# Optimization experiments

Hardware: AMD Instinct MI355X
Metric: run time of the kernel (lower is better)

Reference implementation:

```python
import jax, jax.numpy as jnp
import numpy as np

D_MODEL = 512
NUM_HEADS = 8
D_HEAD = 64
B, T = 8, 1024


def sinusoidal_pos(start, end, d, dtype=jnp.float32):
    # positions start .. end-1, standard sinusoidal encoding, shape (1, end-start, d)
    pos = jnp.arange(start, end, dtype=jnp.float32)[:, None]              # (L,1)
    inv_freq = jnp.exp(-jnp.log(10000.0) * jnp.arange(0, d, 2, dtype=jnp.float32) / d)
    ang = pos * inv_freq[None, :]                                          # (L,d/2)
    pe = jnp.stack([jnp.sin(ang), jnp.cos(ang)], axis=-1).reshape(pos.shape[0], d)
    return pe[None].astype(dtype)                                          # (1,L,d)


def _relative_shift(x):
    # x: (B,H,T,L) -> Transformer-XL shift trick
    b, h, t, l = x.shape
    x = jnp.pad(x, ((0, 0), (0, 0), (0, 0), (1, 0)))                       # (B,H,T,L+1)
    x = x.reshape(b, h, l + 1, t)[:, :, 1:, :].reshape(b, h, t, l)
    return x


def setup_inputs() -> dict:
    key = jax.random.key(0)
    ks = jax.random.split(key, 8)
    hd = NUM_HEADS * D_HEAD
    s_in = 1.0 / np.sqrt(D_MODEL)
    s_out = 1.0 / np.sqrt(hd)
    return {
        "xs": jax.random.normal(ks[0], (B, T, D_MODEL), jnp.float32),
        "mask": jnp.ones((B, T, T), jnp.int32),
        "Wq": jax.random.normal(ks[1], (D_MODEL, hd), jnp.float32) * s_in,
        "Wk": jax.random.normal(ks[2], (D_MODEL, hd), jnp.float32) * s_in,
        "Wv": jax.random.normal(ks[3], (D_MODEL, hd), jnp.float32) * s_in,
        "Wpos": jax.random.normal(ks[4], (D_MODEL, hd), jnp.float32) * s_in,
        "Wout": jax.random.normal(ks[5], (hd, D_MODEL), jnp.float32) * s_out,
        "u_bias": jax.random.normal(ks[6], (NUM_HEADS, D_HEAD), jnp.float32) * 0.02,
        "v_bias": jax.random.normal(ks[7], (NUM_HEADS, D_HEAD), jnp.float32) * 0.02,
    }


def reference(xs, mask, Wq, Wk, Wv, Wpos, Wout, u_bias, v_bias):
    b, t, _ = xs.shape
    scale = 1.0 / np.sqrt(D_HEAD)

    def split_heads(y):  # (B,T,H*dh) -> (B,H,T,dh)
        return y.reshape(b, t, NUM_HEADS, D_HEAD).transpose(0, 2, 1, 3)

    q = split_heads(xs @ Wq)
    k = split_heads(xs @ Wk)
    v = split_heads(xs @ Wv)

    # positions -(T-1) .. T-1, length 2T-1
    pos_enc = sinusoidal_pos(-(t - 1), t, D_MODEL, xs.dtype)               # (1,L,D)
    p = (pos_enc[0] @ Wpos).reshape(-1, NUM_HEADS, D_HEAD).transpose(1, 0, 2)  # (H,L,dh)

    q_u = q + u_bias[None, :, None, :]
    q_v = q + v_bias[None, :, None, :]

    matrix_ac = jnp.einsum("bhtd,bhsd->bhts", q_u, k)                      # (B,H,T,T)
    matrix_bd = jnp.einsum("bhtd,hld->bhtl", q_v, p)                       # (B,H,T,2T-1)
    matrix_bd = _relative_shift(matrix_bd)[:, :, :, :t]                    # (B,H,T,T)

    scores = (matrix_ac + matrix_bd) * scale

    m = (mask[:, None, :, :] == 0)                                          # (B,1,T,T)
    scores = jnp.where(m, -jnp.inf, scores)
    attn = jax.nn.softmax(scores, axis=-1)
    attn = jnp.where(m, 0.0, attn)
    # dropout is identity in eval mode

    z = jnp.einsum("bhts,bhsd->bthd", attn, v).reshape(b, t, NUM_HEADS * D_HEAD)
    return z @ Wout
```

## Files before the change

### kernel.cpp

```cpp
#include <hip/hip_runtime.h>
#include <hip/hip_bf16.h>


typedef unsigned short u16;
typedef unsigned long long u64;
typedef __attribute__((ext_vector_type(8))) short bf16x8;
typedef __attribute__((ext_vector_type(8))) unsigned short ushort8v;
typedef __attribute__((ext_vector_type(4))) float floatx4;

__device__ __forceinline__ float b2f(u16 u) {
    union { unsigned int i; float f; } x; x.i = ((unsigned int)u) << 16; return x.f;
}
__device__ __forceinline__ u16 f2b(float f) {
    __hip_bfloat16 h = __float2bfloat16(f);
    return *reinterpret_cast<u16*>(&h);
}

#define MFMA16(a, b, c) __builtin_amdgcn_mfma_f32_16x16x32_bf16(a, b, c, 0, 0, 0)

__global__ __launch_bounds__(256) void prep_kernel(
    const float* __restrict__ X, u16* __restrict__ Xb,
    const float* __restrict__ W0, const float* __restrict__ W1,
    const float* __restrict__ W2, const float* __restrict__ W3,
    const float* __restrict__ W4, u16* __restrict__ WT,
    const int* __restrict__ mask, u64* __restrict__ Mp,
    u16* __restrict__ Peb)
{
    const int bi = blockIdx.x;
    const int tid = threadIdx.x;
    if (bi < 2048) {
        size_t i = ((size_t)bi * 256 + tid) * 8;
        float4 a = *(const float4*)&X[i];
        float4 b = *(const float4*)&X[i + 4];
        ushort8v s;
        s[0] = f2b(a.x); s[1] = f2b(a.y); s[2] = f2b(a.z); s[3] = f2b(a.w);
        s[4] = f2b(b.x); s[5] = f2b(b.y); s[6] = f2b(b.z); s[7] = f2b(b.w);
        *(ushort8v*)&Xb[i] = s;
    } else if (bi < 2368) {
        __shared__ float t[64][68];
        const int li = bi - 2048;
        const int m = li >> 6;
        const float* src = (m == 0) ? W0 : (m == 1) ? W1 : (m == 2) ? W2
                         : (m == 3) ? W3 : W4;
        u16* dst = WT + (size_t)m * 262144;
        const int sub = li & 63;
        const int k0 = ((sub >> 3) & 7) * 64, n0 = (sub & 7) * 64;
        const int r = tid >> 4, c = tid & 15;
#pragma unroll
        for (int rr = 0; rr < 64; rr += 16) {
            float4 v = *(const float4*)&src[(size_t)(k0 + r + rr) * 512 + n0 + 4 * c];
            t[r + rr][4 * c + 0] = v.x;
            t[r + rr][4 * c + 1] = v.y;
            t[r + rr][4 * c + 2] = v.z;
            t[r + rr][4 * c + 3] = v.w;
        }
        __syncthreads();
        const int nrow = tid >> 2, kc = (tid & 3) * 16;
        ushort8v s0, s1;
#pragma unroll
        for (int e = 0; e < 8; ++e) {
            s0[e] = f2b(t[kc + e][nrow]);
            s1[e] = f2b(t[kc + 8 + e][nrow]);
        }
        *(ushort8v*)&dst[(size_t)(n0 + nrow) * 512 + k0 + kc] = s0;
        *(ushort8v*)&dst[(size_t)(n0 + nrow) * 512 + k0 + kc + 8] = s1;
    } else if (bi < 4416) {
        const int lane = tid & 63, w = tid >> 6;
        const int row = (bi - 2368) * 4 + w;
#pragma unroll
        for (int j = 0; j < 16; ++j) {
            int v = mask[(size_t)row * 1024 + j * 64 + lane];
            u64 bits = __ballot(v != 0);
            if (lane == j) Mp[(size_t)row * 16 + j] = bits;
        }
    } else {
        const int lane = tid & 63, w = tid >> 6;
        const int l = (bi - 4416) * 4 + w;
        const int lc = (l > 2046) ? 2046 : l;
        const float pos = (float)(lc - 1023);
        ushort8v s;
#pragma unroll
        for (int e = 0; e < 8; ++e) {
            int k = (lane << 3) + e;
            int i = k >> 1;
            float invf = expf(-0.035977892f * (float)i);
            float ang = pos * invf;
            float v = (k & 1) ? cosf(ang) : sinf(ang);
            s[e] = f2b(v);
        }
        *(ushort8v*)&Peb[(size_t)l * 512 + (lane << 3)] = s;
    }
}

__global__ __launch_bounds__(256, 2) void qkv_mfma(
    const u16* __restrict__ Xb, const u16* __restrict__ WqT,
    const u16* __restrict__ WkT, const u16* __restrict__ WvT,
    const u16* __restrict__ Peb, const u16* __restrict__ WposT,
    u16* __restrict__ Qb, u16* __restrict__ Kb, u16* __restrict__ Vtg,
    u16* __restrict__ Pg)
{
    __shared__ u16 Xl[128 * 40];
    __shared__ u16 Wl[128 * 40];
    const int tid = threadIdx.x;
    const int lane = tid & 63, w = tid >> 6;
    const int quad = lane >> 4, ln = lane & 15;
    const int wm = w & 1, wn = w >> 1;

    const int yy = blockIdx.y;
    int sel, m0, n0;
    const u16 *Ap, *Bp;
    if (yy < 12) {
        sel = yy >> 2; n0 = (yy & 3) * 128; m0 = blockIdx.x * 128;
        Ap = Xb; Bp = (sel == 0) ? WqT : (sel == 1) ? WkT : WvT;
    } else {
        sel = 3; m0 = (blockIdx.x >> 2) * 128; n0 = (blockIdx.x & 3) * 128;
        Ap = Peb; Bp = WposT;
    }
    const int b = (m0 >> 10) & 7, tbase = m0 & 1023;

    const int sr = tid >> 2, sg = tid & 3;

    floatx4 acc[4][4];
#pragma unroll
    for (int i = 0; i < 4; ++i)
#pragma unroll
        for (int j = 0; j < 4; ++j) acc[i][j] = (floatx4){0.f, 0.f, 0.f, 0.f};

    ushort8v xq[2], wq2[2];
#pragma unroll
    for (int it = 0; it < 2; ++it) {
        int r = sr + it * 64;
        xq[it]  = *(const ushort8v*)&Ap[(size_t)(m0 + r) * 512 + sg * 8];
        wq2[it] = *(const ushort8v*)&Bp[(size_t)(n0 + r) * 512 + sg * 8];
    }

    for (int kc = 0; kc < 512; kc += 32) {
        __syncthreads();
#pragma unroll
        for (int it = 0; it < 2; ++it) {
            int r = sr + it * 64;
            *(ushort8v*)&Xl[r * 40 + sg * 8] = xq[it];
            *(ushort8v*)&Wl[r * 40 + sg * 8] = wq2[it];
        }
        __syncthreads();
        if (kc + 32 < 512) {
#pragma unroll
            for (int it = 0; it < 2; ++it) {
                int r = sr + it * 64;
                xq[it]  = *(const ushort8v*)&Ap[(size_t)(m0 + r) * 512 + kc + 32 + sg * 8];
                wq2[it] = *(const ushort8v*)&Bp[(size_t)(n0 + r) * 512 + kc + 32 + sg * 8];
            }
        }
        bf16x8 am[4], an[4];
#pragma unroll
        for (int i = 0; i < 4; ++i)
            am[i] = *(bf16x8*)&Xl[(wm * 64 + i * 16 + ln) * 40 + quad * 8];
#pragma unroll
        for (int j = 0; j < 4; ++j)
            an[j] = *(bf16x8*)&Wl[(wn * 64 + j * 16 + ln) * 40 + quad * 8];
        if (sel != 2) {
#pragma unroll
            for (int i = 0; i < 4; ++i)
#pragma unroll
                for (int j = 0; j < 4; ++j)
                    acc[i][j] = MFMA16(an[j], am[i], acc[i][j]);
        } else {
#pragma unroll
            for (int i = 0; i < 4; ++i)
#pragma unroll
                for (int j = 0; j < 4; ++j)
                    acc[i][j] = MFMA16(am[i], an[j], acc[i][j]);
        }
    }
    if (sel < 2) {
        u16* dst = (sel == 0) ? Qb : Kb;
#pragma unroll
        for (int i = 0; i < 4; ++i) {
            int t = tbase + wm * 64 + i * 16 + ln;
#pragma unroll
            for (int j = 0; j < 4; ++j) {
                int n = n0 + wn * 64 + j * 16 + quad * 4;
                int h = n >> 6, d = n & 63;
                ushort4 s;
                s.x = f2b(acc[i][j][0]); s.y = f2b(acc[i][j][1]);
                s.z = f2b(acc[i][j][2]); s.w = f2b(acc[i][j][3]);
                *(ushort4*)&dst[(((size_t)b * 8 + h) * 1024 + t) * 64 + d] = s;
            }
        }
    } else if (sel == 2) {
#pragma unroll
        for (int i = 0; i < 4; ++i) {
            int t4 = tbase + wm * 64 + i * 16 + quad * 4;
#pragma unroll
            for (int j = 0; j < 4; ++j) {
                int n = n0 + wn * 64 + j * 16 + ln;
                int h = n >> 6, d = n & 63;
                ushort4 s;
                s.x = f2b(acc[i][j][0]); s.y = f2b(acc[i][j][1]);
                s.z = f2b(acc[i][j][2]); s.w = f2b(acc[i][j][3]);
                *(ushort4*)&Vtg[(((size_t)b * 8 + h) * 64 + d) * 1024 + t4] = s;
            }
        }
    } else {
#pragma unroll
        for (int i = 0; i < 4; ++i) {
            int l = m0 + wm * 64 + i * 16 + ln;
#pragma unroll
            for (int j = 0; j < 4; ++j) {
                int n = n0 + wn * 64 + j * 16 + quad * 4;
                int h = n >> 6, d = n & 63;
                ushort4 s;
                s.x = f2b(acc[i][j][0]); s.y = f2b(acc[i][j][1]);
                s.z = f2b(acc[i][j][2]); s.w = f2b(acc[i][j][3]);
                *(ushort4*)&Pg[(((size_t)h << 11) + l) * 64 + d] = s;
            }
        }
    }
}

__device__ __forceinline__ bf16x8 addbias(bf16x8 q, const float* __restrict__ bias) {
    float4 a = *(const float4*)&bias[0];
    float4 b = *(const float4*)&bias[4];
    bf16x8 r;
    r[0] = (short)f2b(b2f((u16)q[0]) + a.x);
    r[1] = (short)f2b(b2f((u16)q[1]) + a.y);
    r[2] = (short)f2b(b2f((u16)q[2]) + a.z);
    r[3] = (short)f2b(b2f((u16)q[3]) + a.w);
    r[4] = (short)f2b(b2f((u16)q[4]) + b.x);
    r[5] = (short)f2b(b2f((u16)q[5]) + b.y);
    r[6] = (short)f2b(b2f((u16)q[6]) + b.z);
    r[7] = (short)f2b(b2f((u16)q[7]) + b.w);
    return r;
}

__global__ __launch_bounds__(256, 2) void attn_mfma(
    const u16* __restrict__ Qb,
    const u16* __restrict__ Kb, const u16* __restrict__ Vtg,
    const u16* __restrict__ P, const u64* __restrict__ Mp,
    const float* __restrict__ ub, const float* __restrict__ vb,
    u16* __restrict__ Z)
{
    __shared__ u16 Klds[64 * 72];
    __shared__ u16 Vtlds[64 * 72];
    __shared__ u16 Pb[192 * 64];
    __shared__ __align__(16) char WaveBuf[4][16 * 80 * 4];

    const int tid  = threadIdx.x;
    const int lane = tid & 63;
    const int w    = tid >> 6;
    const int quad = lane >> 4;
    const int ln   = lane & 15;

    const int bid = blockIdx.x;
    const int xg  = bid & 7;
    const int idx = bid >> 3;
    const int bh_i = xg * 8 + (idx >> 3);
    const int t0 = (idx & 7) << 7;
    const int h  = bh_i & 7;
    const int b  = bh_i >> 3;
    const size_t bh  = (size_t)bh_i * 1024;
    const size_t bhd = (size_t)bh_i * 64;
    size_t mprow[2];
    mprow[0] = ((size_t)b * 1024 + t0 + 16 * w + ln) * 16;
    mprow[1] = ((size_t)b * 1024 + t0 + 64 + 16 * w + ln) * 16;

    bf16x8 qu0[2], qu1[2], qv0[2], qv1[2];
#pragma unroll
    for (int c = 0; c < 2; ++c) {
        const size_t qoff = (bh + t0 + 64 * c + 16 * w + ln) * 64;
        bf16x8 q0 = *(const bf16x8*)&Qb[qoff + quad * 8];
        bf16x8 q1 = *(const bf16x8*)&Qb[qoff + 32 + quad * 8];
        qu0[c] = addbias(q0, &ub[h * 64 + quad * 8]);
        qu1[c] = addbias(q1, &ub[h * 64 + 32 + quad * 8]);
        qv0[c] = addbias(q0, &vb[h * 64 + quad * 8]);
        qv1[c] = addbias(q1, &vb[h * 64 + 32 + quad * 8]);
    }

    floatx4 O[2][4];
#pragma unroll
    for (int c = 0; c < 2; ++c)
#pragma unroll
        for (int dt = 0; dt < 4; ++dt) O[c][dt] = (floatx4){0.f, 0.f, 0.f, 0.f};
    float m_run[2] = {-3.0e38f, -3.0e38f}, l_run[2] = {0.f, 0.f};

    float* gw = (float*)&WaveBuf[w][0];
    u16*  pw  = (u16*)&WaveBuf[w][0];

    const int str = tid >> 3, stg = tid & 7;
    ushort8v kq[2], vq[2], pq[6];

#define LOAD_CHUNK(S0)                                                            \
    {                                                                             \
        _Pragma("unroll")                                                         \
        for (int it = 0; it < 2; ++it) {                                          \
            int r = str + it * 32;                                                \
            kq[it] = *(const ushort8v*)&Kb[(bh + (S0) + r) * 64 + stg * 8];       \
            vq[it] = *(const ushort8v*)&Vtg[(bhd + r) * 1024 + (S0) + stg * 8];   \
        }                                                                         \
        const int lb0 = 896 - t0 + (S0);                                          \
        _Pragma("unroll")                                                         \
        for (int it = 0; it < 6; ++it) {                                          \
            int r = str + it * 32;                                                \
            size_t l = (size_t)(lb0 + r);                                         \
            pq[it] = *(const ushort8v*)&P[((((size_t)h << 11) + l) << 6) + stg * 8]; \
        }                                                                         \
    }

    LOAD_CHUNK(0)

    for (int s0 = 0; s0 < 1024; s0 += 64) {
        __syncthreads();
#pragma unroll
        for (int it = 0; it < 2; ++it) {
            int r = str + it * 32;
            *(ushort8v*)&Klds[r * 72 + stg * 8] = kq[it];
            *(ushort8v*)&Vtlds[r * 72 + stg * 8] = vq[it];
        }
#pragma unroll
        for (int it = 0; it < 6; ++it) {
            int r = str + it * 32;
            *(ushort8v*)&Pb[r * 64 + ((stg ^ (r & 7)) << 3)] = pq[it];
        }
        __syncthreads();
        if (s0 + 64 < 1024) LOAD_CHUNK(s0 + 64)

        bf16x8 vf0[4], vf1[4];
#pragma unroll
        for (int dt = 0; dt < 4; ++dt) {
            int vr = dt * 16 + ln;
            vf0[dt] = *(bf16x8*)&Vtlds[vr * 72 + quad * 8];
            vf1[dt] = *(bf16x8*)&Vtlds[vr * 72 + 32 + quad * 8];
        }

#pragma unroll
        for (int c = 0; c < 2; ++c) {
            const u64 bits = Mp[mprow[c] + (s0 >> 6)];
            const int rb0 = 112 - 64 * c - 16 * w;
#pragma unroll
            for (int jt = 0; jt < 5; ++jt) {
                int rb = rb0 + jt * 16 + ln;
                bf16x8 a0 = *(bf16x8*)&Pb[rb * 64 + ((quad ^ (rb & 7)) << 3)];
                bf16x8 a1 = *(bf16x8*)&Pb[rb * 64 + (((4 + quad) ^ (rb & 7)) << 3)];
                floatx4 g = {0.f, 0.f, 0.f, 0.f};
                g = MFMA16(a0, qv0[c], g);
                g = MFMA16(a1, qv1[c], g);
                *(floatx4*)&gw[ln * 80 + jt * 16 + quad * 4] = g;
            }
            floatx4 cac[4];
#pragma unroll
            for (int st = 0; st < 4; ++st) {
                int kr = st * 16 + ln;
                bf16x8 a0 = *(bf16x8*)&Klds[kr * 72 + quad * 8];
                bf16x8 a1 = *(bf16x8*)&Klds[kr * 72 + 32 + quad * 8];
                floatx4 cc = {0.f, 0.f, 0.f, 0.f};
                cc = MFMA16(a0, qu0[c], cc);
                cc = MFMA16(a1, qu1[c], cc);
                cac[st] = cc;
            }
            float sc[4][4];
            float cmax = -3.0e38f;
#pragma unroll
            for (int st = 0; st < 4; ++st) {
                int j0 = st * 16 + quad * 4 + 15 - ln;
#pragma unroll
                for (int r = 0; r < 4; ++r) {
                    float v = (cac[st][r] + gw[ln * 80 + j0 + r]) * 0.125f;
                    int ss = st * 16 + quad * 4 + r;
                    v = ((bits >> ss) & 1ull) ? v : -1.0e30f;
                    sc[st][r] = v;
                    cmax = fmaxf(cmax, v);
                }
            }
            cmax = fmaxf(cmax, __shfl_xor(cmax, 16));
            cmax = fmaxf(cmax, __shfl_xor(cmax, 32));
            float m_new = fmaxf(m_run[c], cmax);
            float alpha = __expf(m_run[c] - m_new);
            float psum = 0.f;
#pragma unroll
            for (int st = 0; st < 4; ++st) {
                float p0 = __expf(sc[st][0] - m_new);
                float p1 = __expf(sc[st][1] - m_new);
                float p2 = __expf(sc[st][2] - m_new);
                float p3 = __expf(sc[st][3] - m_new);
                psum += (p0 + p1) + (p2 + p3);
                ushort4 pk;
                pk.x = f2b(p0); pk.y = f2b(p1); pk.z = f2b(p2); pk.w = f2b(p3);
                *(ushort4*)&pw[ln * 72 + st * 16 + quad * 4] = pk;
            }
            psum += __shfl_xor(psum, 16);
            psum += __shfl_xor(psum, 32);
            l_run[c] = l_run[c] * alpha + psum;
            m_run[c] = m_new;
            float a0s = __shfl(alpha, quad * 4 + 0);
            float a1s = __shfl(alpha, quad * 4 + 1);
            float a2s = __shfl(alpha, quad * 4 + 2);
            float a3s = __shfl(alpha, quad * 4 + 3);
#pragma unroll
            for (int dt = 0; dt < 4; ++dt) {
                O[c][dt][0] *= a0s; O[c][dt][1] *= a1s;
                O[c][dt][2] *= a2s; O[c][dt][3] *= a3s;
            }
            bf16x8 pa0 = *(bf16x8*)&pw[ln * 72 + quad * 8];
            bf16x8 pa1 = *(bf16x8*)&pw[ln * 72 + 32 + quad * 8];
#pragma unroll
            for (int dt = 0; dt < 4; ++dt) {
                O[c][dt] = MFMA16(pa0, vf0[dt], O[c][dt]);
                O[c][dt] = MFMA16(pa1, vf1[dt], O[c][dt]);
            }
        }
    }
#pragma unroll
    for (int c = 0; c < 2; ++c) {
        float li[4];
#pragma unroll
        for (int r = 0; r < 4; ++r) li[r] = 1.0f / __shfl(l_run[c], quad * 4 + r);
#pragma unroll
        for (int r = 0; r < 4; ++r) {
            size_t zo = ((size_t)b * 1024 + t0 + 64 * c + 16 * w + quad * 4 + r) * 512
                      + h * 64 + ln;
            Z[zo + 0]  = f2b(O[c][0][r] * li[r]);
            Z[zo + 16] = f2b(O[c][1][r] * li[r]);
            Z[zo + 32] = f2b(O[c][2][r] * li[r]);
            Z[zo + 48] = f2b(O[c][3][r] * li[r]);
        }
    }
}

__global__ __launch_bounds__(256, 2) void out_mfma(
    const u16* __restrict__ Zb, const u16* __restrict__ WoT,
    float* __restrict__ out)
{
    __shared__ u16 Xl[128 * 40];
    __shared__ u16 Wl[128 * 40];
    const int tid = threadIdx.x;
    const int lane = tid & 63, w = tid >> 6;
    const int quad = lane >> 4, ln = lane & 15;
    const int wm = w & 1, wn = w >> 1;
    const int m0 = blockIdx.x * 128;
    const int n0 = blockIdx.y * 128;
    const int sr = tid >> 2, sg = tid & 3;

    floatx4 acc[4][4];
#pragma unroll
    for (int i = 0; i < 4; ++i)
#pragma unroll
        for (int j = 0; j < 4; ++j) acc[i][j] = (floatx4){0.f, 0.f, 0.f, 0.f};

    ushort8v xq[2], wq2[2];
#pragma unroll
    for (int it = 0; it < 2; ++it) {
        int r = sr + it * 64;
        xq[it]  = *(const ushort8v*)&Zb[(size_t)(m0 + r) * 512 + sg * 8];
        wq2[it] = *(const ushort8v*)&WoT[(size_t)(n0 + r) * 512 + sg * 8];
    }

    for (int kc = 0; kc < 512; kc += 32) {
        __syncthreads();
#pragma unroll
        for (int it = 0; it < 2; ++it) {
            int r = sr + it * 64;
            *(ushort8v*)&Xl[r * 40 + sg * 8] = xq[it];
            *(ushort8v*)&Wl[r * 40 + sg * 8] = wq2[it];
        }
        __syncthreads();
        if (kc + 32 < 512) {
#pragma unroll
            for (int it = 0; it < 2; ++it) {
                int r = sr + it * 64;
                xq[it]  = *(const ushort8v*)&Zb[(size_t)(m0 + r) * 512 + kc + 32 + sg * 8];
                wq2[it] = *(const ushort8v*)&WoT[(size_t)(n0 + r) * 512 + kc + 32 + sg * 8];
            }
        }
        bf16x8 am[4], an[4];
#pragma unroll
        for (int i = 0; i < 4; ++i)
            am[i] = *(bf16x8*)&Xl[(wm * 64 + i * 16 + ln) * 40 + quad * 8];
#pragma unroll
        for (int j = 0; j < 4; ++j)
            an[j] = *(bf16x8*)&Wl[(wn * 64 + j * 16 + ln) * 40 + quad * 8];
#pragma unroll
        for (int i = 0; i < 4; ++i)
#pragma unroll
            for (int j = 0; j < 4; ++j)
                acc[i][j] = MFMA16(an[j], am[i], acc[i][j]);
    }
#pragma unroll
    for (int i = 0; i < 4; ++i) {
        int m = m0 + wm * 64 + i * 16 + ln;
#pragma unroll
        for (int j = 0; j < 4; ++j) {
            int n = n0 + wn * 64 + j * 16 + quad * 4;
            float4 s;
            s.x = acc[i][j][0]; s.y = acc[i][j][1];
            s.z = acc[i][j][2]; s.w = acc[i][j][3];
            *(float4*)&out[(size_t)m * 512 + n] = s;
        }
    }
}

extern "C" void kernel_launch(void* const* d_in, const int* in_sizes, int n_in,
                              void* d_out, int out_size, void* d_ws, size_t ws_size,
                              hipStream_t stream) {
    const float* xs   = (const float*)d_in[0];
    const int*   mask = (const int*)d_in[1];
    const float* Wq   = (const float*)d_in[2];
    const float* Wk   = (const float*)d_in[3];
    const float* Wv   = (const float*)d_in[4];
    const float* Wpos = (const float*)d_in[5];
    const float* Wout = (const float*)d_in[6];
    const float* ub   = (const float*)d_in[7];
    const float* vb   = (const float*)d_in[8];
    float* out = (float*)d_out;

    u16* Qb  = (u16*)d_ws;
    u16* Kb  = Qb + 4194304;
    u16* Vtg = Kb + 4194304;
    u16* Pg  = Vtg + 4194304;
    u16* XZ  = Pg + 1048576;
    u16* WT  = XZ + 4194304;
    u16* WqT = WT;
    u16* WkT = WT + 262144;
    u16* WvT = WT + 524288;
    u16* WoT = WT + 786432;
    u16* WposT = WT + 1048576;
    u16* Peb = WT + 1310720;
    u64* Mp  = (u64*)(Peb + 1048576);

    prep_kernel<<<4928, 256, 0, stream>>>(xs, XZ, Wq, Wk, Wv, Wout, Wpos, WT,
                                          mask, Mp, Peb);
    qkv_mfma<<<dim3(64, 13), 256, 0, stream>>>(XZ, WqT, WkT, WvT, Peb, WposT,
                                               Qb, Kb, Vtg, Pg);
    attn_mfma<<<512, 256, 0, stream>>>(Qb, Kb, Vtg, Pg, Mp, ub, vb, XZ);
    out_mfma<<<dim3(64, 4), 256, 0, stream>>>(XZ, WoT, out);
}
```

Measured before the change: 233.4 us.

## Load K/V fragments directly from global and double-buffer P tile in LDS

K and V^T tiles are no longer staged through shared memory; each wave loads its MFMA fragments straight from global memory (relying on L1/L2 reuse across waves). The positional P tile moves to a two-slot LDS buffer, which removes one __syncthreads per iteration. This cuts LDS traffic and barriers but adds redundant global loads across the four waves, and those loads sit directly before the MFMAs with little prefetch to hide their latency.

```diff
diff --git a/kernel.cpp b/kernel.cpp
--- a/kernel.cpp
+++ b/kernel.cpp
@@ -240,9 +240,7 @@
     const float* __restrict__ ub, const float* __restrict__ vb,
     u16* __restrict__ Z)
 {
-    __shared__ u16 Klds[64 * 72];
-    __shared__ u16 Vtlds[64 * 72];
-    __shared__ u16 Pb[192 * 64];
+    __shared__ u16 Pb[2][192 * 64];
     __shared__ __align__(16) char WaveBuf[4][16 * 80 * 4];
 
     const int tid  = threadIdx.x;
@@ -287,60 +285,60 @@
     u16*  pw  = (u16*)&WaveBuf[w][0];
 
     const int str = tid >> 3, stg = tid & 7;
-    ushort8v kq[2], vq[2], pq[6];
-
-#define LOAD_CHUNK(S0)                                                            \
-    {                                                                             \
-        _Pragma("unroll")                                                         \
-        for (int it = 0; it < 2; ++it) {                                          \
-            int r = str + it * 32;                                                \
-            kq[it] = *(const ushort8v*)&Kb[(bh + (S0) + r) * 64 + stg * 8];       \
-            vq[it] = *(const ushort8v*)&Vtg[(bhd + r) * 1024 + (S0) + stg * 8];   \
-        }                                                                         \
-        const int lb0 = 896 - t0 + (S0);                                          \
-        _Pragma("unroll")                                                         \
-        for (int it = 0; it < 6; ++it) {                                          \
-            int r = str + it * 32;                                                \
-            size_t l = (size_t)(lb0 + r);                                         \
-            pq[it] = *(const ushort8v*)&P[((((size_t)h << 11) + l) << 6) + stg * 8]; \
-        }                                                                         \
-    }
-
-    LOAD_CHUNK(0)
-
-    for (int s0 = 0; s0 < 1024; s0 += 64) {
-        __syncthreads();
-#pragma unroll
-        for (int it = 0; it < 2; ++it) {
-            int r = str + it * 32;
-            *(ushort8v*)&Klds[r * 72 + stg * 8] = kq[it];
-            *(ushort8v*)&Vtlds[r * 72 + stg * 8] = vq[it];
-        }
+    ushort8v pq[6];
+
+    {
+        const int lb0 = 896 - t0;
 #pragma unroll
         for (int it = 0; it < 6; ++it) {
             int r = str + it * 32;
-            *(ushort8v*)&Pb[r * 64 + ((stg ^ (r & 7)) << 3)] = pq[it];
+            pq[it] = *(const ushort8v*)&P[((((size_t)h << 11) + (size_t)(lb0 + r)) << 6) + stg * 8];
+        }
+    }
+
+    for (int i = 0; i < 16; ++i) {
+        const int s0 = i << 6;
+        u16* pb = &Pb[i & 1][0];
+
+#pragma unroll
+        for (int it = 0; it < 6; ++it) {
+            int r = str + it * 32;
+            *(ushort8v*)&pb[r * 64 + ((stg ^ (r & 7)) << 3)] = pq[it];
         }
         __syncthreads();
-        if (s0 + 64 < 1024) LOAD_CHUNK(s0 + 64)
-
-        bf16x8 vf0[4], vf1[4];
+
+        if (i < 15) {
+            const int lb0 = 896 - t0 + s0 + 64;
+#pragma unroll
+            for (int it = 0; it < 6; ++it) {
+                int r = str + it * 32;
+                pq[it] = *(const ushort8v*)&P[((((size_t)h << 11) + (size_t)(lb0 + r)) << 6) + stg * 8];
+            }
+        }
+
+        bf16x8 kf[4][2], vf[4][2];
+#pragma unroll
+        for (int st = 0; st < 4; ++st) {
+            const u16* kp = &Kb[(bh + s0 + st * 16 + ln) * 64 + quad * 8];
+            kf[st][0] = *(const bf16x8*)(kp);
+            kf[st][1] = *(const bf16x8*)(kp + 32);
+        }
 #pragma unroll
         for (int dt = 0; dt < 4; ++dt) {
-            int vr = dt * 16 + ln;
-            vf0[dt] = *(bf16x8*)&Vtlds[vr * 72 + quad * 8];
-            vf1[dt] = *(bf16x8*)&Vtlds[vr * 72 + 32 + quad * 8];
+            const u16* vp = &Vtg[(bhd + dt * 16 + ln) * 1024 + s0 + quad * 8];
+            vf[dt][0] = *(const bf16x8*)(vp);
+            vf[dt][1] = *(const bf16x8*)(vp + 32);
         }
 
 #pragma unroll
         for (int c = 0; c < 2; ++c) {
-            const u64 bits = Mp[mprow[c] + (s0 >> 6)];
+            const u64 bits = Mp[mprow[c] + i];
             const int rb0 = 112 - 64 * c - 16 * w;
 #pragma unroll
             for (int jt = 0; jt < 5; ++jt) {
                 int rb = rb0 + jt * 16 + ln;
-                bf16x8 a0 = *(bf16x8*)&Pb[rb * 64 + ((quad ^ (rb & 7)) << 3)];
-                bf16x8 a1 = *(bf16x8*)&Pb[rb * 64 + (((4 + quad) ^ (rb & 7)) << 3)];
+                bf16x8 a0 = *(bf16x8*)&pb[rb * 64 + ((quad ^ (rb & 7)) << 3)];
+                bf16x8 a1 = *(bf16x8*)&pb[rb * 64 + (((4 + quad) ^ (rb & 7)) << 3)];
                 floatx4 g = {0.f, 0.f, 0.f, 0.f};
                 g = MFMA16(a0, qv0[c], g);
                 g = MFMA16(a1, qv1[c], g);
@@ -349,12 +347,9 @@
             floatx4 cac[4];
 #pragma unroll
             for (int st = 0; st < 4; ++st) {
-                int kr = st * 16 + ln;
-                bf16x8 a0 = *(bf16x8*)&Klds[kr * 72 + quad * 8];
-                bf16x8 a1 = *(bf16x8*)&Klds[kr * 72 + 32 + quad * 8];
                 floatx4 cc = {0.f, 0.f, 0.f, 0.f};
-                cc = MFMA16(a0, qu0[c], cc);
-                cc = MFMA16(a1, qu1[c], cc);
+                cc = MFMA16(kf[st][0], qu0[c], cc);
+                cc = MFMA16(kf[st][1], qu1[c], cc);
                 cac[st] = cc;
             }
             float sc[4][4];
@@ -404,8 +399,8 @@
             bf16x8 pa1 = *(bf16x8*)&pw[ln * 72 + 32 + quad * 8];
 #pragma unroll
             for (int dt = 0; dt < 4; ++dt) {
-                O[c][dt] = MFMA16(pa0, vf0[dt], O[c][dt]);
-                O[c][dt] = MFMA16(pa1, vf1[dt], O[c][dt]);
+                O[c][dt] = MFMA16(pa0, vf[dt][0], O[c][dt]);
+                O[c][dt] = MFMA16(pa1, vf[dt][1], O[c][dt]);
             }
         }
     }
```

Result: slower. 243.1 us (+4.2%).
